# Performance work log

Hardware: AMD Instinct MI355X
Metric: run time of the kernel (lower is better)

## Reference

```python
import jax, jax.numpy as jnp
import numpy as np

N = 4096       # num_nodes (must equal out_features: final div broadcasts [C,N]/[N,1])
IN_F = 1024    # module in_features
OUT_F = 4096   # module out_features == N
F_RAW = 512    # raw node feature dim fed to the in-forward Linear


def setup_inputs() -> dict:
    key = jax.random.key(0)
    ks = jax.random.split(key, 5)
    node_features = jax.random.normal(ks[0], (N, F_RAW), dtype=jnp.float32)
    adjacency_matrix = jax.random.bernoulli(ks[1], 0.004, (N, N)).astype(jnp.float32)
    eye = jnp.eye(N, dtype=jnp.float32)
    A0 = adjacency_matrix * (1.0 - eye)                 # adjacency w/o self loops
    S = (A0 @ A0 + A0) * (1.0 - eye)                    # sibling matrix, zero diag
    mask_hadamard = S[:, None, :]                       # [N,1,N]
    mask_father = adjacency_matrix[:, None, :]          # [N,1,N]
    neighbor_count = jnp.maximum(A0.sum(axis=1, keepdims=True), 1.0)  # [N,1]
    lim = float(1.0 / np.sqrt(F_RAW))
    linear_w = jax.random.uniform(ks[2], (IN_F, F_RAW), minval=-lim, maxval=lim, dtype=jnp.float32)
    linear_b = jax.random.uniform(ks[3], (IN_F,), minval=-lim, maxval=lim, dtype=jnp.float32)
    weight = jax.random.normal(ks[4], (IN_F, OUT_F), dtype=jnp.float32) * float(np.sqrt(2.0 / IN_F))
    return dict(node_features=node_features, adjacency_matrix=adjacency_matrix,
                mask_father=mask_father, neighbor_count=neighbor_count,
                mask_hadamard=mask_hadamard, linear_w=linear_w, linear_b=linear_b,
                weight=weight)


def reference(node_features, adjacency_matrix, mask_father, neighbor_count,
              mask_hadamard, linear_w, linear_b, weight):
    # Linear + projection: wf[n,c]
    x = node_features @ linear_w.T + linear_b           # [N, IN_F]
    wf = x @ weight                                      # [N, C]
    # Original builds masked_hadamard[j,i,c] = wf[i,c]*wf[j,c]*S[i,j] ([N,C,N]),
    # contracts with adjacency over i, masks with adj[k,j], sums over k:
    #   sum_hadamard[c,j] = wf[j,c] * sum_i (sum_k adj[k,j]*adj[k,i]) * S[i,j] * wf[i,c]
    # Fused form avoids the O(N^2 C) intermediates; same math.
    A_out = mask_father[:, 0, :]                         # adj[k,j]  [N,N]
    S = mask_hadamard[:, 0, :]                           # S[i,j]    [N,N]
    G = A_out.T @ adjacency_matrix                       # G[j,i] = sum_k adj[k,j]*adj[k,i]
    P = G * S.T                                          # P[j,i] = G[j,i]*S[i,j]
    sum_hadamard = (wf * (P @ wf)).T                     # [C, N]
    # Final broadcast division exactly as torch: [C,N] / [N,1] (requires C==N)
    return sum_hadamard / jnp.square(neighbor_count)
```

## Files before the change

kernel.cpp:

```cpp
#include <hip/hip_runtime.h>
#include <hip/hip_bf16.h>

typedef __attribute__((ext_vector_type(8))) short s16x8;
typedef __attribute__((ext_vector_type(4))) float f32x4;
typedef __attribute__((ext_vector_type(8))) unsigned short u16x8;

__device__ __forceinline__ float b2f(unsigned short u) {
  union { unsigned int i; float f; } x; x.i = ((unsigned int)u) << 16; return x.f;
}
__device__ __forceinline__ unsigned short f2b(float f) {
  __hip_bfloat16 h = __float2bfloat16(f);
  return *reinterpret_cast<unsigned short*>(&h);
}

#define TILE 128
#define BK 32
#define PCAP 128
#define SCAP 1024

template <int EPI>
__device__ __forceinline__ void gemm_body(
    unsigned short* As, unsigned short* Bs,
    int bx, int by,
    const unsigned short* __restrict__ A,
    const unsigned short* __restrict__ B,
    unsigned short* __restrict__ C,
    int M, int N, int K,
    const float* __restrict__ epi_f)
{
  const int tid  = threadIdx.x;
  const int lane = tid & 63;
  const int wave = tid >> 6;
  const int wm = (wave & 1) * 64;
  const int wn = (wave >> 1) * 64;
  const long bm = (long)by * TILE;
  const long bn = (long)bx * TILE;

  f32x4 acc[4][4] = {};

  auto STAGE = [&](int kt, int b) {
    const long kb = (long)kt * BK;
#pragma unroll
    for (int i = 0; i < 2; ++i) {
      const int c0 = (wave * 2 + i) * 64;
      const int c  = c0 + lane;
      const int r  = c >> 2;
      const int cc = ((c & 3) ^ ((c >> 3) & 3)) * 8;
      const unsigned short* ga = A + (bm + r) * (long)K + kb + cc;
      const unsigned short* gb = B + (bn + r) * (long)K + kb + cc;
      __builtin_amdgcn_global_load_lds(
          (const __attribute__((address_space(1))) void*)ga,
          (__attribute__((address_space(3))) void*)(As + b * (TILE * BK) + c0 * 8), 16, 0, 0);
      __builtin_amdgcn_global_load_lds(
          (const __attribute__((address_space(1))) void*)gb,
          (__attribute__((address_space(3))) void*)(Bs + b * (TILE * BK) + c0 * 8), 16, 0, 0);
    }
  };

  const int kTiles = K / BK;
  STAGE(0, 0);

  for (int kt = 0; kt < kTiles; ++kt) {
    const int cur = kt & 1;
    if (kt + 1 < kTiles) {
      STAGE(kt + 1, cur ^ 1);
      asm volatile("s_waitcnt vmcnt(4)" ::: "memory");
    } else {
      asm volatile("s_waitcnt vmcnt(0)" ::: "memory");
    }
    __builtin_amdgcn_sched_barrier(0);
    __builtin_amdgcn_s_barrier();
    __builtin_amdgcn_sched_barrier(0);

    const int rl = lane & 15;
    const int kqx = ((lane >> 4) ^ ((rl >> 1) & 3)) * 8;
    s16x8 af[4], bfr[4];
#pragma unroll
    for (int mi = 0; mi < 4; ++mi)
      af[mi] = *(const s16x8*)(As + cur * (TILE * BK) + (wm + mi * 16 + rl) * BK + kqx);
#pragma unroll
    for (int ni = 0; ni < 4; ++ni)
      bfr[ni] = *(const s16x8*)(Bs + cur * (TILE * BK) + (wn + ni * 16 + rl) * BK + kqx);
#pragma unroll
    for (int mi = 0; mi < 4; ++mi)
#pragma unroll
      for (int ni = 0; ni < 4; ++ni)
        acc[mi][ni] = __builtin_amdgcn_mfma_f32_16x16x32_bf16(af[mi], bfr[ni], acc[mi][ni], 0, 0, 0);

    __builtin_amdgcn_sched_barrier(0);
    __builtin_amdgcn_s_barrier();
    __builtin_amdgcn_sched_barrier(0);
  }

  const int cl = lane & 15;
  const int rq = (lane >> 4) * 4;
#pragma unroll
  for (int mi = 0; mi < 4; ++mi)
#pragma unroll
    for (int ni = 0; ni < 4; ++ni)
#pragma unroll
      for (int r = 0; r < 4; ++r) {
        const long row = bm + wm + mi * 16 + rq + r;
        const long col = bn + wn + ni * 16 + cl;
        float v = acc[mi][ni][r];
        if (EPI == 1) v += epi_f[col];
        C[row * (long)N + col] = f2b(v);
      }
}

template <int EPI>
__global__ __launch_bounds__(256) void gemm_nt(
    const unsigned short* __restrict__ A,
    const unsigned short* __restrict__ B,
    unsigned short* __restrict__ C,
    int M, int N, int K,
    const float* __restrict__ epi_f)
{
  __shared__ unsigned short As[2 * TILE * BK];
  __shared__ unsigned short Bs[2 * TILE * BK];
  gemm_body<EPI>(As, Bs, blockIdx.x, blockIdx.y, A, B, C, M, N, K, epi_f);
}

__device__ __forceinline__ void colbits_body(
    int i, const float* __restrict__ adj, unsigned long long* __restrict__ colb)
{
  const int t = threadIdx.x;
  const unsigned long long bit = 1ull << (i & 63);
  const int w = i >> 6;
  const float* r = adj + (long)i * 4096;
#pragma unroll
  for (int q = 0; q < 4; ++q) {
    int c = (t + q * 256) * 4;
    float4 v = *(const float4*)(r + c);
    if (v.x != 0.f) atomicOr(&colb[(long)(c + 0) * 64 + w], bit);
    if (v.y != 0.f) atomicOr(&colb[(long)(c + 1) * 64 + w], bit);
    if (v.z != 0.f) atomicOr(&colb[(long)(c + 2) * 64 + w], bit);
    if (v.w != 0.f) atomicOr(&colb[(long)(c + 3) * 64 + w], bit);
  }
}

__global__ __launch_bounds__(256) void build_P2(
    const float* __restrict__ S, const unsigned long long* __restrict__ colb,
    int* __restrict__ pk, float* __restrict__ pv, int* __restrict__ pcnt)
{
  const int k = blockIdx.x;
  const int t = threadIdx.x;
  const int lane = t & 63;
  __shared__ __align__(16) unsigned long long ck[64];
  __shared__ int jl[SCAP];
  __shared__ float sl[SCAP];
  __shared__ int m;
  if (t == 0) m = 0;
  if (t < 64) ck[t] = colb[(long)k * 64 + t];
  __syncthreads();
  const float* Sr = S + (long)k * 4096;
  const unsigned long long lmask = (1ull << lane) - 1ull;
#pragma unroll
  for (int q = 0; q < 4; ++q) {
    int c = (t + q * 256) * 4;
    float4 v = *(const float4*)(Sr + c);
    float vals[4] = { v.x, v.y, v.z, v.w };
#pragma unroll
    for (int r = 0; r < 4; ++r) {
      float vv = vals[r];
      unsigned long long mask = __ballot(vv != 0.f);
      if (mask) {
        int base;
        if (lane == 0) base = atomicAdd(&m, __popcll(mask));
        base = __shfl(base, 0, 64);
        if (vv != 0.f) {
          int pos = base + __popcll(mask & lmask);
          if (pos < SCAP) { jl[pos] = c + r; sl[pos] = vv; }
        }
      }
    }
  }
  __syncthreads();
  const int mm = min(m, SCAP);
  const int l = t & 7;
  for (int idx = (t >> 3); idx < mm; idx += 32) {
    const int j = jl[idx];
    const ulonglong2* cj = (const ulonglong2*)(colb + (long)j * 64);
    int cnt = 0;
#pragma unroll
    for (int it = 0; it < 4; ++it) {
      ulonglong2 q  = cj[it * 8 + l];
      ulonglong2 cc = *(const ulonglong2*)&ck[it * 16 + l * 2];
      cnt += __popcll(q.x & cc.x) + __popcll(q.y & cc.y);
    }
    cnt += __shfl_down(cnt, 4, 8);
    cnt += __shfl_down(cnt, 2, 8);
    cnt += __shfl_down(cnt, 1, 8);
    if (l == 0 && cnt > 0) {
      int slot = atomicAdd(&pcnt[j], 1);
      if (slot < PCAP) {
        pk[(long)j * PCAP + slot] = k;
        pv[(long)j * PCAP + slot] = (float)cnt * sl[idx];
      }
    }
  }
}

__global__ __launch_bounds__(256) void prep_fused(
    const float* __restrict__ w,  unsigned short* __restrict__ weightT,
    const float* __restrict__ nf, unsigned short* __restrict__ nfb,
    const float* __restrict__ lw, unsigned short* __restrict__ lwb,
    float* __restrict__ zp)
{
  __shared__ unsigned short tile[64][66];
  const int b = blockIdx.x;
  const int t = threadIdx.x;
  if (b < 1024) {
    const int R = 1024, C = 4096;
    const long r0 = (long)(b >> 6) * 64;
    const long c0 = (long)(b & 63) * 64;
#pragma unroll
    for (int i = 0; i < 4; ++i) {
      int v = t + i * 256;
      int r = v >> 4;
      int c = (v & 15) * 4;
      float4 d = *(const float4*)(w + (r0 + r) * (long)C + c0 + c);
      tile[r][c + 0] = f2b(d.x); tile[r][c + 1] = f2b(d.y);
      tile[r][c + 2] = f2b(d.z); tile[r][c + 3] = f2b(d.w);
    }
    __syncthreads();
#pragma unroll
    for (int i = 0; i < 4; ++i) {
      int v = t + i * 256;
      int r = v >> 4;
      int c = (v & 15) * 4;
      ushort4 d;
      d.x = tile[c + 0][r]; d.y = tile[c + 1][r]; d.z = tile[c + 2][r]; d.w = tile[c + 3][r];
      *(ushort4*)(weightT + (c0 + r) * (long)R + r0 + c) = d;
    }
  } else if (b < 3072) {
    const long e = ((long)(b - 1024) * 256 + t) * 4;
    float4 d = *(const float4*)(nf + e);
    ushort4 o;
    o.x = f2b(d.x); o.y = f2b(d.y); o.z = f2b(d.z); o.w = f2b(d.w);
    *(ushort4*)(nfb + e) = o;
  } else if (b < 3584) {
    const long e = ((long)(b - 3072) * 256 + t) * 4;
    float4 d = *(const float4*)(lw + e);
    ushort4 o;
    o.x = f2b(d.x); o.y = f2b(d.y); o.z = f2b(d.z); o.w = f2b(d.w);
    *(ushort4*)(lwb + e) = o;
  } else {
    const long e = ((long)(b - 3584) * 256 + t) * 4;
    *(float4*)(zp + e) = make_float4(0.f, 0.f, 0.f, 0.f);
  }
}

__global__ __launch_bounds__(256) void g1_colbits(
    const unsigned short* __restrict__ nfb, const unsigned short* __restrict__ lwb,
    unsigned short* __restrict__ x, const float* __restrict__ lb,
    const float* __restrict__ adj, unsigned long long* __restrict__ colb)
{
  extern __shared__ ulonglong2 dsm[];
  const int b = blockIdx.x;
  if (b < 256) {
    unsigned short* As = (unsigned short*)dsm;
    unsigned short* Bs = As + 2 * TILE * BK;
    gemm_body<1>(As, Bs, b & 7, b >> 3, nfb, lwb, x, 4096, 1024, 512, lb);
  } else {
    colbits_body(b - 256, adj, colb);
  }
}

__global__ __launch_bounds__(256) void spmm_fused(
    const int* __restrict__ pk, const float* __restrict__ pv,
    const int* __restrict__ pcnt, const unsigned short* __restrict__ wf,
    const float* __restrict__ nc, float* __restrict__ VO)
{
  __shared__ int   k_l[4][PCAP];
  __shared__ float v_l[4][PCAP];
  __shared__ int   n_s[4];
  const int t = threadIdx.x;
  const int wave = t >> 6;
  const int lane = t & 63;
  const int seg = blockIdx.x;
  const int jb  = blockIdx.y * 4;
  {
    int e0 = t;
    k_l[e0 >> 7][e0 & 127] = pk[(long)(jb + (e0 >> 7)) * PCAP + (e0 & 127)];
    v_l[e0 >> 7][e0 & 127] = pv[(long)(jb + (e0 >> 7)) * PCAP + (e0 & 127)];
    int e1 = t + 256;
    k_l[e1 >> 7][e1 & 127] = pk[(long)(jb + (e1 >> 7)) * PCAP + (e1 & 127)];
    v_l[e1 >> 7][e1 & 127] = pv[(long)(jb + (e1 >> 7)) * PCAP + (e1 & 127)];
    if (t < 4) n_s[t] = min(pcnt[jb + t], PCAP);
  }
  __syncthreads();
  const int j = jb + wave;
  const int n = n_s[wave];
  const int* __restrict__ kk = k_l[wave];
  const float* __restrict__ vv = v_l[wave];
  const int c0 = seg * 512 + lane * 8;

  float acc[8] = {};
  int m = 0;
  for (; m + 8 <= n; m += 8) {
    float vs[8];
    u16x8 d[8];
#pragma unroll
    for (int r = 0; r < 8; ++r) {
      vs[r] = vv[m + r];
      d[r] = *(const u16x8*)(wf + (unsigned)(kk[m + r] * 4096 + c0));
    }
    __builtin_amdgcn_sched_barrier(0);
#pragma unroll
    for (int r = 0; r < 8; ++r)
#pragma unroll
      for (int q = 0; q < 8; ++q)
        acc[q] += vs[r] * b2f(d[r][q]);
  }
  for (; m + 2 <= n; m += 2) {
    const float v0 = vv[m], v1 = vv[m + 1];
    u16x8 a = *(const u16x8*)(wf + (unsigned)(kk[m]     * 4096 + c0));
    u16x8 b = *(const u16x8*)(wf + (unsigned)(kk[m + 1] * 4096 + c0));
#pragma unroll
    for (int q = 0; q < 8; ++q) acc[q] += v0 * b2f(a[q]) + v1 * b2f(b[q]);
  }
  for (; m < n; ++m) {
    const float va = vv[m];
    u16x8 a = *(const u16x8*)(wf + (unsigned)(kk[m] * 4096 + c0));
#pragma unroll
    for (int q = 0; q < 8; ++q) acc[q] += va * b2f(a[q]);
  }
  u16x8 wa = *(const u16x8*)(wf + (unsigned)(j * 4096 + c0));
  float out[8];
#pragma unroll
  for (int q = 0; q < 8; q += 4) {
    float4 nv = *(const float4*)(nc + c0 + q);
    float n4[4] = { nv.x, nv.y, nv.z, nv.w };
#pragma unroll
    for (int r = 0; r < 4; ++r)
      out[q + r] = acc[q + r] * b2f(wa[q + r]) / (n4[r] * n4[r]);
  }
  float* dst = VO + (long)j * 4096 + c0;
  *(float4*)(dst + 0) = make_float4(out[0], out[1], out[2], out[3]);
  *(float4*)(dst + 4) = make_float4(out[4], out[5], out[6], out[7]);
}

__global__ __launch_bounds__(256) void final_transpose(float* __restrict__ D)
{
  const int bx = blockIdx.x, by = blockIdx.y;
  if (by > bx) return;
  const int X = bx * 64, Y = by * 64;
  const bool diag = (bx == by);
  __shared__ float t1[64][65];
  __shared__ float t2[64][65];
  const int t = threadIdx.x;
  const int r0 = t >> 4;
  const int c4 = (t & 15) * 4;
#pragma unroll
  for (int i = 0; i < 4; ++i) {
    int r = r0 + i * 16;
    float4 d = *(const float4*)&D[(long)(Y + r) * 4096 + X + c4];
    t1[r][c4 + 0] = d.x; t1[r][c4 + 1] = d.y; t1[r][c4 + 2] = d.z; t1[r][c4 + 3] = d.w;
    if (!diag) {
      float4 e = *(const float4*)&D[(long)(X + r) * 4096 + Y + c4];
      t2[r][c4 + 0] = e.x; t2[r][c4 + 1] = e.y; t2[r][c4 + 2] = e.z; t2[r][c4 + 3] = e.w;
    }
  }
  __syncthreads();
#pragma unroll
  for (int i = 0; i < 4; ++i) {
    int r = r0 + i * 16;
    float4 o;
    o.x = t1[c4 + 0][r]; o.y = t1[c4 + 1][r]; o.z = t1[c4 + 2][r]; o.w = t1[c4 + 3][r];
    *(float4*)&D[(long)(X + r) * 4096 + Y + c4] = o;
    if (!diag) {
      float4 p;
      p.x = t2[c4 + 0][r]; p.y = t2[c4 + 1][r]; p.z = t2[c4 + 2][r]; p.w = t2[c4 + 3][r];
      *(float4*)&D[(long)(Y + r) * 4096 + X + c4] = p;
    }
  }
}

extern "C" void kernel_launch(void* const* d_in, const int* in_sizes, int n_in,
                              void* d_out, int out_size, void* d_ws, size_t ws_size,
                              hipStream_t stream) {
  const float* nf  = (const float*)d_in[0];
  const float* adj = (const float*)d_in[1];
  const float* nc  = (const float*)d_in[3];
  const float* S   = (const float*)d_in[4];
  const float* lw  = (const float*)d_in[5];
  const float* lb  = (const float*)d_in[6];
  const float* w   = (const float*)d_in[7];

  char* ws = (char*)d_ws;
  unsigned short*      wf      = (unsigned short*)(ws);
  unsigned long long*  colb    = (unsigned long long*)(ws + (32ll << 20));
  int*                 pcnt    = (int*)(ws + (34ll << 20));
  int*                 pk      = (int*)(ws + (35ll << 20));
  float*               pv      = (float*)(ws + (37ll << 20));
  unsigned short*      weightT = (unsigned short*)(ws + (40ll << 20));
  unsigned short*      nfb     = (unsigned short*)(ws + (48ll << 20));
  unsigned short*      lwb     = (unsigned short*)(ws + (52ll << 20));
  unsigned short*      x       = (unsigned short*)(ws + (54ll << 20));
  float*               VO      = (float*)d_out;

  prep_fused<<<4100, 256, 0, stream>>>(w, weightT, nf, nfb, lw, lwb, (float*)colb);
  g1_colbits<<<4352, 256, 32768, stream>>>(nfb, lwb, x, lb, adj, colb);
  build_P2<<<4096, 256, 0, stream>>>(S, colb, pk, pv, pcnt);
  gemm_nt<0><<<dim3(32, 32), 256, 0, stream>>>(x, weightT, wf, 4096, 4096, 1024, nullptr);
  spmm_fused<<<dim3(8, 1024), 256, 0, stream>>>(pk, pv, pcnt, wf, nc, VO);
  final_transpose<<<dim3(64, 64), 256, 0, stream>>>(VO);
}
```

Before: 377.4 us.

## Reassociate linear and projection into precomputed combined weight W2

Rewrites wf = (nf·Lwᵀ + b)·W as nf·(Lwᵀ·W) + b·W. A small GEMM now builds a combined 512x4096 weight and a bias vector b2 = b·W, and the big GEMM runs with K=512 instead of K=1024. This removes about half the FLOPs of the large projection GEMM and drops the intermediate x matrix. It adds a transpose of linear_w, a naive per-column bias reduction in the prep kernel, and an extra bf16 rounding of the combined weight.

```diff
diff --git a/kernel.cpp b/kernel.cpp
--- a/kernel.cpp
+++ b/kernel.cpp
@@ -201,69 +201,82 @@
   }
 }
 
+__device__ __forceinline__ void transpose64_f2b(
+    const float* __restrict__ in, unsigned short* __restrict__ out,
+    int R, int C, long r0, long c0, unsigned short (*tile)[66])
+{
+  const int t = threadIdx.x;
+#pragma unroll
+  for (int i = 0; i < 4; ++i) {
+    int v = t + i * 256;
+    int r = v >> 4;
+    int c = (v & 15) * 4;
+    float4 d = *(const float4*)(in + (r0 + r) * (long)C + c0 + c);
+    tile[r][c + 0] = f2b(d.x); tile[r][c + 1] = f2b(d.y);
+    tile[r][c + 2] = f2b(d.z); tile[r][c + 3] = f2b(d.w);
+  }
+  __syncthreads();
+#pragma unroll
+  for (int i = 0; i < 4; ++i) {
+    int v = t + i * 256;
+    int r = v >> 4;
+    int c = (v & 15) * 4;
+    ushort4 d;
+    d.x = tile[c + 0][r]; d.y = tile[c + 1][r]; d.z = tile[c + 2][r]; d.w = tile[c + 3][r];
+    *(ushort4*)(out + (c0 + r) * (long)R + r0 + c) = d;
+  }
+}
+
 __global__ __launch_bounds__(256) void prep_fused(
     const float* __restrict__ w,  unsigned short* __restrict__ weightT,
     const float* __restrict__ nf, unsigned short* __restrict__ nfb,
-    const float* __restrict__ lw, unsigned short* __restrict__ lwb,
-    float* __restrict__ zp)
+    const float* __restrict__ lw, unsigned short* __restrict__ lwbT,
+    float* __restrict__ zp,
+    const float* __restrict__ lb, float* __restrict__ b2)
 {
   __shared__ unsigned short tile[64][66];
   const int b = blockIdx.x;
   const int t = threadIdx.x;
   if (b < 1024) {
-    const int R = 1024, C = 4096;
-    const long r0 = (long)(b >> 6) * 64;
-    const long c0 = (long)(b & 63) * 64;
-#pragma unroll
-    for (int i = 0; i < 4; ++i) {
-      int v = t + i * 256;
-      int r = v >> 4;
-      int c = (v & 15) * 4;
-      float4 d = *(const float4*)(w + (r0 + r) * (long)C + c0 + c);
-      tile[r][c + 0] = f2b(d.x); tile[r][c + 1] = f2b(d.y);
-      tile[r][c + 2] = f2b(d.z); tile[r][c + 3] = f2b(d.w);
-    }
-    __syncthreads();
-#pragma unroll
-    for (int i = 0; i < 4; ++i) {
-      int v = t + i * 256;
-      int r = v >> 4;
-      int c = (v & 15) * 4;
-      ushort4 d;
-      d.x = tile[c + 0][r]; d.y = tile[c + 1][r]; d.z = tile[c + 2][r]; d.w = tile[c + 3][r];
-      *(ushort4*)(weightT + (c0 + r) * (long)R + r0 + c) = d;
-    }
+    transpose64_f2b(w, weightT, 1024, 4096, (long)(b >> 6) * 64, (long)(b & 63) * 64, tile);
   } else if (b < 3072) {
     const long e = ((long)(b - 1024) * 256 + t) * 4;
     float4 d = *(const float4*)(nf + e);
     ushort4 o;
     o.x = f2b(d.x); o.y = f2b(d.y); o.z = f2b(d.z); o.w = f2b(d.w);
     *(ushort4*)(nfb + e) = o;
-  } else if (b < 3584) {
-    const long e = ((long)(b - 3072) * 256 + t) * 4;
-    float4 d = *(const float4*)(lw + e);
-    ushort4 o;
-    o.x = f2b(d.x); o.y = f2b(d.y); o.z = f2b(d.z); o.w = f2b(d.w);
-    *(ushort4*)(lwb + e) = o;
+  } else if (b < 3200) {
+    const int idx = b - 3072;
+    transpose64_f2b(lw, lwbT, 1024, 512, (long)(idx >> 3) * 64, (long)(idx & 7) * 64, tile);
+  } else if (b < 3716) {
+    const long e = ((long)(b - 3200) * 256 + t) * 4;
+    *(float4*)(zp + e) = make_float4(0.f, 0.f, 0.f, 0.f);
   } else {
-    const long e = ((long)(b - 3584) * 256 + t) * 4;
-    *(float4*)(zp + e) = make_float4(0.f, 0.f, 0.f, 0.f);
-  }
-}
-
-__global__ __launch_bounds__(256) void g1_colbits(
-    const unsigned short* __restrict__ nfb, const unsigned short* __restrict__ lwb,
-    unsigned short* __restrict__ x, const float* __restrict__ lb,
+    const int n = (b - 3716) * 256 + t;
+    float acc = 0.f;
+    for (int k = 0; k < 1024; k += 4) {
+      acc += lb[k]     * w[(long)k * 4096 + n]
+           + lb[k + 1] * w[(long)(k + 1) * 4096 + n]
+           + lb[k + 2] * w[(long)(k + 2) * 4096 + n]
+           + lb[k + 3] * w[(long)(k + 3) * 4096 + n];
+    }
+    b2[n] = acc;
+  }
+}
+
+__global__ __launch_bounds__(256) void gw2_colbits(
+    const unsigned short* __restrict__ weightT, const unsigned short* __restrict__ lwbT,
+    unsigned short* __restrict__ W2T,
     const float* __restrict__ adj, unsigned long long* __restrict__ colb)
 {
   extern __shared__ ulonglong2 dsm[];
   const int b = blockIdx.x;
-  if (b < 256) {
+  if (b < 128) {
     unsigned short* As = (unsigned short*)dsm;
     unsigned short* Bs = As + 2 * TILE * BK;
-    gemm_body<1>(As, Bs, b & 7, b >> 3, nfb, lwb, x, 4096, 1024, 512, lb);
+    gemm_body<0>(As, Bs, b & 3, b >> 2, weightT, lwbT, W2T, 4096, 512, 1024, nullptr);
   } else {
-    colbits_body(b - 256, adj, colb);
+    colbits_body(b - 128, adj, colb);
   }
 }
 
@@ -396,14 +409,15 @@
   float*               pv      = (float*)(ws + (37ll << 20));
   unsigned short*      weightT = (unsigned short*)(ws + (40ll << 20));
   unsigned short*      nfb     = (unsigned short*)(ws + (48ll << 20));
-  unsigned short*      lwb     = (unsigned short*)(ws + (52ll << 20));
-  unsigned short*      x       = (unsigned short*)(ws + (54ll << 20));
+  unsigned short*      lwbT    = (unsigned short*)(ws + (52ll << 20));
+  unsigned short*      W2T     = (unsigned short*)(ws + (54ll << 20));
+  float*               b2      = (float*)(ws + (58ll << 20));
   float*               VO      = (float*)d_out;
 
-  prep_fused<<<4100, 256, 0, stream>>>(w, weightT, nf, nfb, lw, lwb, (float*)colb);
-  g1_colbits<<<4352, 256, 32768, stream>>>(nfb, lwb, x, lb, adj, colb);
+  prep_fused<<<3732, 256, 0, stream>>>(w, weightT, nf, nfb, lw, lwbT, (float*)colb, lb, b2);
+  gw2_colbits<<<4224, 256, 32768, stream>>>(weightT, lwbT, W2T, adj, colb);
   build_P2<<<4096, 256, 0, stream>>>(S, colb, pk, pv, pcnt);
-  gemm_nt<0><<<dim3(32, 32), 256, 0, stream>>>(x, weightT, wf, 4096, 4096, 1024, nullptr);
+  gemm_nt<1><<<dim3(32, 32), 256, 0, stream>>>(nfb, W2T, wf, 4096, 4096, 512, b2);
   spmm_fused<<<dim3(8, 1024), 256, 0, stream>>>(pk, pv, pcnt, wf, nc, VO);
   final_transpose<<<dim3(64, 64), 256, 0, stream>>>(VO);
 }
```

Measured after the change: 387.5 us. 1.03x slower.
